# Kernel tuning notes

Hardware: AMD Instinct MI355X
Metric: run time of the kernel (lower is better)

## Reference

```python
import jax, jax.numpy as jnp
import numpy as np

# Hyperparameters (from HOIMLoss init_kwargs / defaults)
NUM_PIDS = 5532
NUM_CQ = 5000
NUM_BG = 5000
NUM_FEATURES = 256
BATCH = 4096
OIM_SCALAR = 30.0
ALPHA_D = 0.25
ALPHA_R = 0.25
GAMMA_D = 2.0
GAMMA_R = 2.0


def _l2norm(x):
    return x / jnp.maximum(jnp.linalg.norm(x, axis=-1, keepdims=True), 1e-12)


def setup_inputs() -> dict:
    key = jax.random.key(0)
    k1, k2, k3, k4, k5 = jax.random.split(key, 5)
    inputs = _l2norm(jax.random.normal(k1, (BATCH, NUM_FEATURES), dtype=jnp.float32))
    # roi_label: -2 = background, -1 = ignored unlabeled, [0, NUM_PIDS) = identity
    roi_label = jax.random.randint(k2, (BATCH,), -2, NUM_PIDS)
    lut = _l2norm(jax.random.normal(k3, (NUM_PIDS, NUM_FEATURES), dtype=jnp.float32))
    cq = _l2norm(jax.random.normal(k4, (NUM_CQ, NUM_FEATURES), dtype=jnp.float32))
    cqb = _l2norm(jax.random.normal(k5, (NUM_BG, NUM_FEATURES), dtype=jnp.float32))
    return {"inputs": inputs, "roi_label": roi_label, "lut": lut, "cq": cq, "cqb": cqb}


def reference(inputs, roi_label, lut, cq, cqb):
    # OIM2CQ.forward: concat([inputs@cqb.T, inputs@lut.T, inputs@cq.T], dim=1)
    table = jnp.concatenate([cqb, lut, cq], axis=0)        # [BG+P+CQ, F]
    projected = OIM_SCALAR * (inputs @ table.T)            # [B, BG+P+CQ]

    valid = roi_label >= -1      # non-background rows (inds in torch code)
    labeled = roi_label >= 0     # rows contributing to nll (ignore_index=-1)

    # OIM focal loss over non-background columns [labeled | unlabeled]
    proj_non_bg = projected[:, NUM_BG:]                    # [B, P+CQ]
    logp = jax.nn.log_softmax(proj_non_bg, axis=-1)
    p = jnp.exp(logp)
    focal_p = ALPHA_R * (1.0 - p) ** GAMMA_R * logp
    safe_lab = jnp.clip(roi_label, 0, NUM_PIDS - 1)
    row_loss = -jnp.take_along_axis(focal_p, safe_lab[:, None], axis=1)[:, 0]
    row_loss = jnp.where(labeled, row_loss, 0.0)           # ignore_index=-1 -> 0

    # Detection focal loss over (background, foreground) mass
    all_probs = jax.nn.softmax(projected, axis=-1)
    cls_score = jnp.stack(
        [all_probs[:, :NUM_BG].sum(axis=-1), all_probs[:, NUM_BG:].sum(axis=-1)],
        axis=-1,
    )                                                      # [B, 2]
    det_label = jnp.clip(roi_label + 2, 0, 1)              # -2 -> 0, else 1
    focal_det = ALPHA_D * (1.0 - cls_score) ** GAMMA_D * jnp.log(cls_score)
    loss_det = -jnp.take_along_axis(focal_det, det_label[:, None], axis=1)[:, 0].mean()

    # dynamic_lambda: weight per-row oim loss by detached fg prob squared
    cls_non_bg = jax.lax.stop_gradient(cls_score[:, 1])
    row_loss = row_loss * cls_non_bg ** 2
    n_valid = jnp.maximum(valid.sum(), 1).astype(projected.dtype)
    loss_oim = jnp.sum(jnp.where(valid, row_loss, 0.0)) / n_valid

    return cls_score, loss_det, loss_oim
```

## Files before the change

kernel.cpp:

```cpp
#include <hip/hip_runtime.h>
#include <hip/hip_bf16.h>

typedef unsigned short u16;
typedef __attribute__((ext_vector_type(8))) short bf16x8;
typedef __attribute__((ext_vector_type(4))) short bf16x4;
typedef __attribute__((ext_vector_type(4))) float f32x4;

#define NBG   5000
#define NPID  5532
#define NTOT  15532
#define FEAT  256
#define BATCH 4096
#define SCALE_LOG2E 43.280851226668994f
#define LPITCH 264

#define NTILE_B  976
#define TILE_SH  4096
#define NTILE_A  256

#define TABT_BYTES ((size_t)NTILE_B * TILE_SH * 2)
#define AT_BYTES   ((size_t)NTILE_A * TILE_SH * 2)
#define SUMS_OFF   (TABT_BYTES + AT_BYTES)
#define SUMS_FLOATS 8196
#define WS_NEED    (SUMS_OFF + SUMS_FLOATS * 4)

__device__ __forceinline__ void atomic_add_f(float* p, float v) {
    __hip_atomic_fetch_add(p, v, __ATOMIC_RELAXED, __HIP_MEMORY_SCOPE_AGENT);
}
__device__ __forceinline__ short f2bf(float f) {
    return (short)__bfloat16_as_ushort(__float2bfloat16(f));
}

__device__ __forceinline__ const float* table_row(
    int n, const float* __restrict__ lut, const float* __restrict__ cq,
    const float* __restrict__ cqb)
{
    const int nc = n < NTOT ? n : NTOT - 1;
    if (nc < NBG)        return cqb + (size_t)nc * FEAT;
    if (nc < NBG + NPID) return lut + (size_t)(nc - NBG) * FEAT;
    return cq + (size_t)(nc - NBG - NPID) * FEAT;
}

#define TAB_UNITS (NTILE_B * 512)
#define A_UNITS   (NTILE_A * 512)
#define PRE_BLOCKS ((TAB_UNITS + A_UNITS) / 256)

__global__ __launch_bounds__(256) void prepass_kernel(
    const float* __restrict__ inputs, const float* __restrict__ lut,
    const float* __restrict__ cq, const float* __restrict__ cqb,
    u16* __restrict__ tabt, u16* __restrict__ at, float* __restrict__ S)
{
    const int u = blockIdx.x * 256 + threadIdx.x;
    if (u < SUMS_FLOATS) S[u] = 0.f;

    if (u < TAB_UNITS) {
        const int tile = u >> 9, v = u & 511;
        const int kk = v >> 6, col = (v >> 2) & 15, q = v & 3;
        const int cg = tile * 16 + col;
        bf16x8 r = {0, 0, 0, 0, 0, 0, 0, 0};
        if (cg < NTOT) {
            const float* src = table_row(cg, lut, cq, cqb) + kk * 32 + q * 8;
            const f32x4 lo = *(const f32x4*)src;
            const f32x4 hi = *(const f32x4*)(src + 4);
            r = bf16x8{ f2bf(lo[0]), f2bf(lo[1]), f2bf(lo[2]), f2bf(lo[3]),
                        f2bf(hi[0]), f2bf(hi[1]), f2bf(hi[2]), f2bf(hi[3]) };
        }
        *(bf16x8*)(tabt + (size_t)u * 8) = r;
    } else {
        const int ua = u - TAB_UNITS;
        const int tile = ua >> 9, v = ua & 511;
        const int kk = v >> 6, row = (v >> 2) & 15, q = v & 3;
        const float* src = inputs + (size_t)(tile * 16 + row) * FEAT + kk * 32 + q * 8;
        const f32x4 lo = *(const f32x4*)src;
        const f32x4 hi = *(const f32x4*)(src + 4);
        bf16x8 r = { f2bf(lo[0]), f2bf(lo[1]), f2bf(lo[2]), f2bf(lo[3]),
                     f2bf(hi[0]), f2bf(hi[1]), f2bf(hi[2]), f2bf(hi[3]) };
        *(bf16x8*)(at + (size_t)ua * 8) = r;
    }
}

__global__ __launch_bounds__(256, 2) void score_bf16_kernel(
    const u16* __restrict__ tabt, const u16* __restrict__ at,
    float* __restrict__ sum_bg, float* __restrict__ sum_nb)
{
    __shared__ __align__(16) short lbuf[2][TILE_SH];
    const int lid = blockIdx.x;
    const int x8  = lid & 7;
    const int j   = lid >> 3;
    const int rowchunk = x8 * 2 + (j & 1);
    const int colchunk = j >> 1;

    const int tid  = threadIdx.x;
    const int wave = tid >> 6;
    const int lane = tid & 63;
    const int l15  = lane & 15;
    const int quad = lane >> 4;

    bf16x8 af[4][8];
    {
        const u16* ab = at + (size_t)(rowchunk * 16 + wave * 4) * TILE_SH
                           + l15 * 32 + quad * 8;
        #pragma unroll
        for (int s = 0; s < 4; ++s)
            #pragma unroll
            for (int kk = 0; kk < 8; ++kk)
                af[s][kk] = *(const bf16x8*)(ab + (size_t)s * TILE_SH + kk * 512);
    }

    float pbg[16], pnb[16];
    #pragma unroll
    for (int i = 0; i < 16; ++i) { pbg[i] = 0.f; pnb[i] = 0.f; }

    const int bt0  = colchunk * 16;
    const int tmax = (colchunk == 60) ? 11 : 16;

    bf16x8 r0, r1;
    {
        const u16* g = tabt + (size_t)bt0 * TILE_SH;
        r0 = *(const bf16x8*)(g + tid * 8);
        r1 = *(const bf16x8*)(g + 2048 + tid * 8);
    }

    #pragma unroll 1
    for (int t = 0; t < tmax; ++t) {
        const int bt = bt0 + t;
        {
            short* dst = lbuf[t & 1];
            *(bf16x8*)(dst + tid * 8) = r0;
            *(bf16x8*)(dst + 2048 + tid * 8) = r1;
        }
        if (t + 1 < tmax) {
            const u16* g = tabt + (size_t)(bt + 1) * TILE_SH;
            r0 = *(const bf16x8*)(g + tid * 8);
            r1 = *(const bf16x8*)(g + 2048 + tid * 8);
        }
        __syncthreads();

        const short* lb = lbuf[t & 1];
        f32x4 cc[4];
        #pragma unroll
        for (int s = 0; s < 4; ++s) cc[s] = f32x4{0.f, 0.f, 0.f, 0.f};
        #pragma unroll
        for (int kk = 0; kk < 8; ++kk) {
            const bf16x8 b = *(const bf16x8*)(lb + kk * 512 + l15 * 32 + quad * 8);
            cc[0] = __builtin_amdgcn_mfma_f32_16x16x32_bf16(af[0][kk], b, cc[0], 0, 0, 0);
            cc[1] = __builtin_amdgcn_mfma_f32_16x16x32_bf16(af[1][kk], b, cc[1], 0, 0, 0);
            cc[2] = __builtin_amdgcn_mfma_f32_16x16x32_bf16(af[2][kk], b, cc[2], 0, 0, 0);
            cc[3] = __builtin_amdgcn_mfma_f32_16x16x32_bf16(af[3][kk], b, cc[3], 0, 0, 0);
        }

        if (colchunk != 60) {
            if (bt < 312) {
                #pragma unroll
                for (int s = 0; s < 4; ++s)
                    #pragma unroll
                    for (int r = 0; r < 4; ++r)
                        pbg[s * 4 + r] += exp2f(cc[s][r] * SCALE_LOG2E);
            } else if (bt > 312) {
                #pragma unroll
                for (int s = 0; s < 4; ++s)
                    #pragma unroll
                    for (int r = 0; r < 4; ++r)
                        pnb[s * 4 + r] += exp2f(cc[s][r] * SCALE_LOG2E);
            } else {
                const bool isbg = l15 < 8;
                #pragma unroll
                for (int s = 0; s < 4; ++s)
                    #pragma unroll
                    for (int r = 0; r < 4; ++r) {
                        const float e = exp2f(cc[s][r] * SCALE_LOG2E);
                        pbg[s * 4 + r] += isbg ? e : 0.f;
                        pnb[s * 4 + r] += isbg ? 0.f : e;
                    }
            }
        } else {
            const bool okc = (bt * 16 + l15) < NTOT;
            #pragma unroll
            for (int s = 0; s < 4; ++s)
                #pragma unroll
                for (int r = 0; r < 4; ++r) {
                    const float e = exp2f(cc[s][r] * SCALE_LOG2E);
                    pnb[s * 4 + r] += okc ? e : 0.f;
                }
        }
    }

    #pragma unroll
    for (int off = 1; off < 16; off <<= 1) {
        #pragma unroll
        for (int i = 0; i < 16; ++i) {
            pbg[i] += __shfl_xor(pbg[i], off);
            pnb[i] += __shfl_xor(pnb[i], off);
        }
    }
    if (l15 == 0) {
        #pragma unroll
        for (int s = 0; s < 4; ++s) {
            #pragma unroll
            for (int r = 0; r < 4; ++r) {
                const int row = (rowchunk * 16 + wave * 4 + s) * 16 + quad * 4 + r;
                atomic_add_f(&sum_bg[row], pbg[s * 4 + r]);
                atomic_add_f(&sum_nb[row], pnb[s * 4 + r]);
            }
        }
    }
}

__global__ __launch_bounds__(256, 2) void score_f32_kernel(
    const float* __restrict__ inputs, const float* __restrict__ lut,
    const float* __restrict__ cq, const float* __restrict__ cqb,
    float* __restrict__ sum_bg, float* __restrict__ sum_nb)
{
    __shared__ __align__(16) short lds[32 * LPITCH];
    const int wave = threadIdx.x >> 6;
    const int lane = threadIdx.x & 63;
    const int l15  = lane & 15;
    const int quad = lane >> 4;
    const int rowbase = blockIdx.y * 256;
    const int colbase = blockIdx.x * 256;

    bf16x8 afrag[4][8];
    #pragma unroll 1
    for (int c = 0; c < 8; ++c) {
        __syncthreads();
        #pragma unroll
        for (int i = 0; i < 8; ++i) {
            const int lr = i * 4 + wave;
            const f32x4 v = *(const f32x4*)(inputs + (size_t)(rowbase + c * 32 + lr) * FEAT + lane * 4);
            bf16x4 h = { f2bf(v[0]), f2bf(v[1]), f2bf(v[2]), f2bf(v[3]) };
            *(bf16x4*)(&lds[lr * LPITCH + lane * 4]) = h;
        }
        __syncthreads();
        if ((c >> 1) == wave) {
            const int half = c & 1;
            #pragma unroll
            for (int j2 = 0; j2 < 2; ++j2) {
                const int lr = j2 * 16 + l15;
                #pragma unroll
                for (int kk = 0; kk < 8; ++kk)
                    afrag[half * 2 + j2][kk] =
                        *(const bf16x8*)(&lds[lr * LPITCH + kk * 32 + quad * 8]);
            }
        }
    }

    float pbg[16], pnb[16];
    #pragma unroll
    for (int i = 0; i < 16; ++i) { pbg[i] = 0.f; pnb[i] = 0.f; }

    #pragma unroll 1
    for (int s = 0; s < 8; ++s) {
        __syncthreads();
        #pragma unroll
        for (int i = 0; i < 8; ++i) {
            const int lc = i * 4 + wave;
            const f32x4 v = *(const f32x4*)(table_row(colbase + s * 32 + lc, lut, cq, cqb) + lane * 4);
            bf16x4 h = { f2bf(v[0]), f2bf(v[1]), f2bf(v[2]), f2bf(v[3]) };
            *(bf16x4*)(&lds[lc * LPITCH + lane * 4]) = h;
        }
        __syncthreads();

        #pragma unroll
        for (int st = 0; st < 2; ++st) {
            const int lc = st * 16 + l15;
            f32x4 cc[4];
            #pragma unroll
            for (int q = 0; q < 4; ++q) cc[q] = f32x4{0.f, 0.f, 0.f, 0.f};
            #pragma unroll
            for (int kk = 0; kk < 8; ++kk) {
                const bf16x8 b = *(const bf16x8*)(&lds[lc * LPITCH + kk * 32 + quad * 8]);
                cc[0] = __builtin_amdgcn_mfma_f32_16x16x32_bf16(afrag[0][kk], b, cc[0], 0, 0, 0);
                cc[1] = __builtin_amdgcn_mfma_f32_16x16x32_bf16(afrag[1][kk], b, cc[1], 0, 0, 0);
                cc[2] = __builtin_amdgcn_mfma_f32_16x16x32_bf16(afrag[2][kk], b, cc[2], 0, 0, 0);
                cc[3] = __builtin_amdgcn_mfma_f32_16x16x32_bf16(afrag[3][kk], b, cc[3], 0, 0, 0);
            }
            const int n = colbase + s * 32 + st * 16 + l15;
            const bool okc  = n < NTOT;
            const bool isbg = n < NBG;
            #pragma unroll
            for (int q = 0; q < 4; ++q) {
                #pragma unroll
                for (int r = 0; r < 4; ++r) {
                    float e = exp2f(cc[q][r] * SCALE_LOG2E);
                    e = okc ? e : 0.f;
                    pbg[q * 4 + r] += isbg ? e : 0.f;
                    pnb[q * 4 + r] += isbg ? 0.f : e;
                }
            }
        }
    }

    #pragma unroll
    for (int off = 1; off < 16; off <<= 1) {
        #pragma unroll
        for (int i = 0; i < 16; ++i) {
            pbg[i] += __shfl_xor(pbg[i], off);
            pnb[i] += __shfl_xor(pnb[i], off);
        }
    }
    if (l15 == 0) {
        #pragma unroll
        for (int q = 0; q < 4; ++q) {
            #pragma unroll
            for (int r = 0; r < 4; ++r) {
                const int row = rowbase + wave * 64 + q * 16 + quad * 4 + r;
                atomic_add_f(&sum_bg[row], pbg[q * 4 + r]);
                atomic_add_f(&sum_nb[row], pnb[q * 4 + r]);
            }
        }
    }
}

__global__ __launch_bounds__(256) void finalize_kernel(
    const float* __restrict__ inputs, const int* __restrict__ roi_label,
    const float* __restrict__ lut,
    const float* __restrict__ sum_bg, const float* __restrict__ sum_nb,
    float* __restrict__ accums, unsigned int* __restrict__ ticket,
    float* __restrict__ out)
{
    __shared__ float s_det[4], s_oim[4], s_nv[4];
    const int wid  = threadIdx.x >> 6;
    const int lane = threadIdx.x & 63;

    float det_a = 0.f, oim_a = 0.f, nv_a = 0.f;

    #pragma unroll 1
    for (int it = 0; it < 8; ++it) {
        const int row = blockIdx.x * 32 + wid * 8 + it;
        const int r   = roi_label[row];

        float dot = 0.f;
        {
            const int rc = r < 0 ? 0 : r;
            const f32x4 xi = *(const f32x4*)(inputs + (size_t)row * FEAT + lane * 4);
            const f32x4 li = *(const f32x4*)(lut + (size_t)rc * FEAT + lane * 4);
            #pragma unroll
            for (int jj = 0; jj < 4; ++jj) {
                float a = __bfloat162float(__float2bfloat16(xi[jj]));
                float b = __bfloat162float(__float2bfloat16(li[jj]));
                dot += a * b;
            }
        }
        #pragma unroll
        for (int off = 32; off > 0; off >>= 1) dot += __shfl_xor(dot, off);

        if (lane == 0) {
            const float sbg = sum_bg[row];
            const float snb = sum_nb[row];
            const float inv = 1.f / (sbg + snb);
            const float cls0 = sbg * inv;
            const float cls1 = snb * inv;
            out[2 * row]     = cls0;
            out[2 * row + 1] = cls1;

            const float cs = (r >= -1) ? cls1 : cls0;
            const float om = 1.f - cs;
            det_a += -(0.25f * om * om * logf(cs)) * (1.f / (float)BATCH);
            nv_a  += (r >= -1) ? 1.f : 0.f;

            if (r >= 0) {
                const float slab = 30.f * dot;
                const float logp = slab - logf(snb);
                const float p    = expf(logp);
                const float om2  = 1.f - p;
                oim_a += -(0.25f * om2 * om2 * logp) * cls1 * cls1;
            }
        }
    }

    if (lane == 0) { s_det[wid] = det_a; s_oim[wid] = oim_a; s_nv[wid] = nv_a; }
    __syncthreads();
    if (threadIdx.x == 0) {
        atomic_add_f(&accums[0], s_det[0] + s_det[1] + s_det[2] + s_det[3]);
        atomic_add_f(&accums[1], s_oim[0] + s_oim[1] + s_oim[2] + s_oim[3]);
        atomic_add_f(&accums[2], s_nv[0] + s_nv[1] + s_nv[2] + s_nv[3]);
        __threadfence();
        const unsigned t = __hip_atomic_fetch_add(ticket, 1u, __ATOMIC_ACQ_REL,
                                                  __HIP_MEMORY_SCOPE_AGENT);
        if (t == gridDim.x - 1) {
            const float det = __hip_atomic_load(&accums[0], __ATOMIC_RELAXED, __HIP_MEMORY_SCOPE_AGENT);
            const float oim = __hip_atomic_load(&accums[1], __ATOMIC_RELAXED, __HIP_MEMORY_SCOPE_AGENT);
            float nv        = __hip_atomic_load(&accums[2], __ATOMIC_RELAXED, __HIP_MEMORY_SCOPE_AGENT);
            if (nv < 1.f) nv = 1.f;
            out[2 * BATCH]     = det;
            out[2 * BATCH + 1] = oim / nv;
        }
    }
}

extern "C" void kernel_launch(void* const* d_in, const int* in_sizes, int n_in,
                              void* d_out, int out_size, void* d_ws, size_t ws_size,
                              hipStream_t stream)
{
    const float* inputs = (const float*)d_in[0];
    const int*   roi    = (const int*)d_in[1];
    const float* lut    = (const float*)d_in[2];
    const float* cq     = (const float*)d_in[3];
    const float* cqb    = (const float*)d_in[4];
    float* out = (float*)d_out;

    if (ws_size >= (size_t)WS_NEED) {
        u16* tabt = (u16*)d_ws;
        u16* at   = (u16*)((char*)d_ws + TABT_BYTES);
        float* S  = (float*)((char*)d_ws + SUMS_OFF);
        prepass_kernel<<<PRE_BLOCKS, 256, 0, stream>>>(inputs, lut, cq, cqb, tabt, at, S);
        score_bf16_kernel<<<976, 256, 0, stream>>>(tabt, at, S, S + BATCH);
        finalize_kernel<<<128, 256, 0, stream>>>(
            inputs, roi, lut, S, S + BATCH, S + 2 * BATCH,
            (unsigned int*)(S + 2 * BATCH + 3), out);
    } else {
        float* S = (float*)d_ws;
        hipMemsetAsync(S, 0, SUMS_FLOATS * sizeof(float), stream);
        dim3 g1(61, 16);
        score_f32_kernel<<<g1, 256, 0, stream>>>(inputs, lut, cq, cqb, S, S + BATCH);
        finalize_kernel<<<128, 256, 0, stream>>>(
            inputs, roi, lut, S, S + BATCH, S + 2 * BATCH,
            (unsigned int*)(S + 2 * BATCH + 3), out);
    }
}
```

Measured before the change: 141.5 us.

## Fold scale into table, swizzle LDS layout, double tiles per sync, raw exp2

Folds the scale*log2e factor into the bf16 table during the prepass, so the score loop can call the hardware exp2 builtin directly without a multiply. Stores both table and input tiles with an XOR swizzle on the 8-element quad to avoid LDS bank conflicts on fragment reads. Stages two column tiles per loop step, which halves the number of barriers and doubles the LDS buffer size. Baking the scale into the bf16 table before rounding slightly changes precision, and the larger LDS footprint may affect occupancy.

Result: faster. 128.7 us (-9.1%).

```diff
diff --git a/kernel.cpp b/kernel.cpp
--- a/kernel.cpp
+++ b/kernel.cpp
@@ -17,6 +17,7 @@
 #define NTILE_B  976
 #define TILE_SH  4096
 #define NTILE_A  256
+#define STEP_SH  8192
 
 #define TABT_BYTES ((size_t)NTILE_B * TILE_SH * 2)
 #define AT_BYTES   ((size_t)NTILE_A * TILE_SH * 2)
@@ -24,12 +25,21 @@
 #define SUMS_FLOATS 8196
 #define WS_NEED    (SUMS_OFF + SUMS_FLOATS * 4)
 
+__device__ __forceinline__ float fexp2(float x) {
+#if __has_builtin(__builtin_amdgcn_exp2f)
+    return __builtin_amdgcn_exp2f(x);
+#else
+    return exp2f(x);
+#endif
+}
+
 __device__ __forceinline__ void atomic_add_f(float* p, float v) {
     __hip_atomic_fetch_add(p, v, __ATOMIC_RELAXED, __HIP_MEMORY_SCOPE_AGENT);
 }
 __device__ __forceinline__ short f2bf(float f) {
     return (short)__bfloat16_as_ushort(__float2bfloat16(f));
 }
+__device__ __forceinline__ int swz(int rc, int q) { return q ^ ((rc >> 1) & 3); }
 
 __device__ __forceinline__ const float* table_row(
     int n, const float* __restrict__ lut, const float* __restrict__ cq,
@@ -62,10 +72,13 @@
             const float* src = table_row(cg, lut, cq, cqb) + kk * 32 + q * 8;
             const f32x4 lo = *(const f32x4*)src;
             const f32x4 hi = *(const f32x4*)(src + 4);
-            r = bf16x8{ f2bf(lo[0]), f2bf(lo[1]), f2bf(lo[2]), f2bf(lo[3]),
-                        f2bf(hi[0]), f2bf(hi[1]), f2bf(hi[2]), f2bf(hi[3]) };
-        }
-        *(bf16x8*)(tabt + (size_t)u * 8) = r;
+            r = bf16x8{ f2bf(lo[0] * SCALE_LOG2E), f2bf(lo[1] * SCALE_LOG2E),
+                        f2bf(lo[2] * SCALE_LOG2E), f2bf(lo[3] * SCALE_LOG2E),
+                        f2bf(hi[0] * SCALE_LOG2E), f2bf(hi[1] * SCALE_LOG2E),
+                        f2bf(hi[2] * SCALE_LOG2E), f2bf(hi[3] * SCALE_LOG2E) };
+        }
+        const size_t off = (size_t)tile * TILE_SH + kk * 512 + col * 32 + swz(col, q) * 8;
+        *(bf16x8*)(tabt + off) = r;
     } else {
         const int ua = u - TAB_UNITS;
         const int tile = ua >> 9, v = ua & 511;
@@ -75,7 +88,8 @@
         const f32x4 hi = *(const f32x4*)(src + 4);
         bf16x8 r = { f2bf(lo[0]), f2bf(lo[1]), f2bf(lo[2]), f2bf(lo[3]),
                      f2bf(hi[0]), f2bf(hi[1]), f2bf(hi[2]), f2bf(hi[3]) };
-        *(bf16x8*)(at + (size_t)ua * 8) = r;
+        const size_t off = (size_t)tile * TILE_SH + kk * 512 + row * 32 + swz(row, q) * 8;
+        *(bf16x8*)(at + off) = r;
     }
 }
 
@@ -83,7 +97,7 @@
     const u16* __restrict__ tabt, const u16* __restrict__ at,
     float* __restrict__ sum_bg, float* __restrict__ sum_nb)
 {
-    __shared__ __align__(16) short lbuf[2][TILE_SH];
+    __shared__ __align__(16) short lbuf[2][STEP_SH];
     const int lid = blockIdx.x;
     const int x8  = lid & 7;
     const int j   = lid >> 3;
@@ -95,11 +109,11 @@
     const int lane = tid & 63;
     const int l15  = lane & 15;
     const int quad = lane >> 4;
+    const int frag_off = l15 * 32 + swz(l15, quad) * 8;
 
     bf16x8 af[4][8];
     {
-        const u16* ab = at + (size_t)(rowchunk * 16 + wave * 4) * TILE_SH
-                           + l15 * 32 + quad * 8;
+        const u16* ab = at + (size_t)(rowchunk * 16 + wave * 4) * TILE_SH + frag_off;
         #pragma unroll
         for (int s = 0; s < 4; ++s)
             #pragma unroll
@@ -111,77 +125,81 @@
     #pragma unroll
     for (int i = 0; i < 16; ++i) { pbg[i] = 0.f; pnb[i] = 0.f; }
 
-    const int bt0  = colchunk * 16;
-    const int tmax = (colchunk == 60) ? 11 : 16;
-
-    bf16x8 r0, r1;
+    const int steps = (colchunk == 60) ? 6 : 8;
+    const u16* gbase = tabt + (size_t)colchunk * 16 * TILE_SH;
+
+    bf16x8 r0, r1, r2, r3;
     {
-        const u16* g = tabt + (size_t)bt0 * TILE_SH;
-        r0 = *(const bf16x8*)(g + tid * 8);
-        r1 = *(const bf16x8*)(g + 2048 + tid * 8);
+        r0 = *(const bf16x8*)(gbase + tid * 8);
+        r1 = *(const bf16x8*)(gbase + 2048 + tid * 8);
+        r2 = *(const bf16x8*)(gbase + 4096 + tid * 8);
+        r3 = *(const bf16x8*)(gbase + 6144 + tid * 8);
     }
 
     #pragma unroll 1
-    for (int t = 0; t < tmax; ++t) {
-        const int bt = bt0 + t;
+    for (int t = 0; t < steps; ++t) {
         {
             short* dst = lbuf[t & 1];
-            *(bf16x8*)(dst + tid * 8) = r0;
+            *(bf16x8*)(dst + tid * 8)        = r0;
             *(bf16x8*)(dst + 2048 + tid * 8) = r1;
-        }
-        if (t + 1 < tmax) {
-            const u16* g = tabt + (size_t)(bt + 1) * TILE_SH;
+            *(bf16x8*)(dst + 4096 + tid * 8) = r2;
+            *(bf16x8*)(dst + 6144 + tid * 8) = r3;
+        }
+        if (t + 1 < steps) {
+            const u16* g = gbase + (size_t)(t + 1) * STEP_SH;
             r0 = *(const bf16x8*)(g + tid * 8);
             r1 = *(const bf16x8*)(g + 2048 + tid * 8);
+            r2 = *(const bf16x8*)(g + 4096 + tid * 8);
+            r3 = *(const bf16x8*)(g + 6144 + tid * 8);
         }
         __syncthreads();
 
         const short* lb = lbuf[t & 1];
-        f32x4 cc[4];
-        #pragma unroll
-        for (int s = 0; s < 4; ++s) cc[s] = f32x4{0.f, 0.f, 0.f, 0.f};
-        #pragma unroll
-        for (int kk = 0; kk < 8; ++kk) {
-            const bf16x8 b = *(const bf16x8*)(lb + kk * 512 + l15 * 32 + quad * 8);
-            cc[0] = __builtin_amdgcn_mfma_f32_16x16x32_bf16(af[0][kk], b, cc[0], 0, 0, 0);
-            cc[1] = __builtin_amdgcn_mfma_f32_16x16x32_bf16(af[1][kk], b, cc[1], 0, 0, 0);
-            cc[2] = __builtin_amdgcn_mfma_f32_16x16x32_bf16(af[2][kk], b, cc[2], 0, 0, 0);
-            cc[3] = __builtin_amdgcn_mfma_f32_16x16x32_bf16(af[3][kk], b, cc[3], 0, 0, 0);
-        }
-
-        if (colchunk != 60) {
-            if (bt < 312) {
+        #pragma unroll
+        for (int h = 0; h < 2; ++h) {
+            const int bt = colchunk * 16 + t * 2 + h;
+            f32x4 cc[4];
+            #pragma unroll
+            for (int s = 0; s < 4; ++s) cc[s] = f32x4{0.f, 0.f, 0.f, 0.f};
+            #pragma unroll
+            for (int kk = 0; kk < 8; ++kk) {
+                const bf16x8 b = *(const bf16x8*)(lb + h * TILE_SH + kk * 512 + frag_off);
+                cc[0] = __builtin_amdgcn_mfma_f32_16x16x32_bf16(af[0][kk], b, cc[0], 0, 0, 0);
+                cc[1] = __builtin_amdgcn_mfma_f32_16x16x32_bf16(af[1][kk], b, cc[1], 0, 0, 0);
+                cc[2] = __builtin_amdgcn_mfma_f32_16x16x32_bf16(af[2][kk], b, cc[2], 0, 0, 0);
+                cc[3] = __builtin_amdgcn_mfma_f32_16x16x32_bf16(af[3][kk], b, cc[3], 0, 0, 0);
+            }
+
+            if (colchunk == 60) {
+                const bool okc = (bt * 16 + l15) < NTOT;
                 #pragma unroll
                 for (int s = 0; s < 4; ++s)
                     #pragma unroll
                     for (int r = 0; r < 4; ++r)
-                        pbg[s * 4 + r] += exp2f(cc[s][r] * SCALE_LOG2E);
-            } else if (bt > 312) {
+                        pnb[s * 4 + r] += okc ? fexp2(cc[s][r]) : 0.f;
+            } else if (bt < 312) {
                 #pragma unroll
                 for (int s = 0; s < 4; ++s)
                     #pragma unroll
                     for (int r = 0; r < 4; ++r)
-                        pnb[s * 4 + r] += exp2f(cc[s][r] * SCALE_LOG2E);
+                        pbg[s * 4 + r] += fexp2(cc[s][r]);
+            } else if (bt > 312) {
+                #pragma unroll
+                for (int s = 0; s < 4; ++s)
+                    #pragma unroll
+                    for (int r = 0; r < 4; ++r)
+                        pnb[s * 4 + r] += fexp2(cc[s][r]);
             } else {
                 const bool isbg = l15 < 8;
                 #pragma unroll
                 for (int s = 0; s < 4; ++s)
                     #pragma unroll
                     for (int r = 0; r < 4; ++r) {
-                        const float e = exp2f(cc[s][r] * SCALE_LOG2E);
+                        const float e = fexp2(cc[s][r]);
                         pbg[s * 4 + r] += isbg ? e : 0.f;
                         pnb[s * 4 + r] += isbg ? 0.f : e;
                     }
             }
-        } else {
-            const bool okc = (bt * 16 + l15) < NTOT;
-            #pragma unroll
-            for (int s = 0; s < 4; ++s)
-                #pragma unroll
-                for (int r = 0; r < 4; ++r) {
-                    const float e = exp2f(cc[s][r] * SCALE_LOG2E);
-                    pnb[s * 4 + r] += okc ? e : 0.f;
-                }
         }
     }
 
```
